# Kernel tuning notes

Hardware: AMD Instinct MI355X
Metric: run time of the kernel (lower is better)

## Reference

```python
import jax, jax.numpy as jnp
import numpy as np

B, D, K = 16384, 256, 1024

def setup_inputs() -> dict:
    key = jax.random.key(0)
    k1, k2 = jax.random.split(key)
    x = jax.random.normal(k1, (B, D), dtype=jnp.float32)
    centers = jax.random.uniform(k2, (K, D), dtype=jnp.float32)  # RandomUniform(0,1)
    betas = jnp.ones((K,), dtype=jnp.float32)
    return {"x": x, "centers": centers, "betas": betas}

def reference(x, centers, betas):
    x_sq = jnp.sum(x * x, axis=-1, keepdims=True)          # [B,1]
    c_sq = jnp.sum(centers * centers, axis=-1)             # [K]
    cross = jnp.einsum('bd,kd->bk', x, centers)            # [B,K]
    diffnorm = x_sq + c_sq[None, :] - 2.0 * cross          # [B,K]
    return jnp.exp(-betas[None, :] * diffnorm)             # [B,K]
```

## Files before the change

### kernel.cpp

```cpp
#include <hip/hip_runtime.h>
#include <stdint.h>

#define D_DIM 256
#define K_CTR 1024
#define B_ROWS 16384
#define BM 32

typedef float f32x4 __attribute__((ext_vector_type(4)));
typedef long long i64x2 __attribute__((ext_vector_type(2)));

static __device__ __forceinline__ unsigned cvt4_fp8(const float4 v) {
    int r = __builtin_amdgcn_cvt_pk_fp8_f32(v.x, v.y, 0, false);
    r = __builtin_amdgcn_cvt_pk_fp8_f32(v.z, v.w, r, true);
    return (unsigned)r;
}

static __device__ __forceinline__ void barrier_lgkm() {
    asm volatile("s_waitcnt lgkmcnt(0)" ::: "memory");
    __builtin_amdgcn_s_barrier();
}

__global__ __launch_bounds__(256) void rbf_prep(const float* __restrict__ centers,
                                                unsigned char* __restrict__ cbf,
                                                float* __restrict__ csq) {
    const int w = threadIdx.x >> 6;
    const int l = threadIdx.x & 63;
    const int c0 = blockIdx.x * 4 + w;
    const float4 v = *reinterpret_cast<const float4*>(centers + c0 * D_DIM + l * 4);
    float s = v.x * v.x + v.y * v.y + v.z * v.z + v.w * v.w;
    const unsigned u = cvt4_fp8(v);
    const unsigned off = (unsigned)((c0 >> 4) * 4096 + (l >> 4) * 1024
                       + (((l >> 1) & 3) * 16 + (c0 & 15)) * 16
                       + ((l >> 3) & 1) * 8 + (l & 1) * 4);
    *reinterpret_cast<unsigned*>(cbf + off) = u;
    #pragma unroll
    for (int off2 = 1; off2 < 64; off2 <<= 1) s += __shfl_xor(s, off2);
    if (l == 0) csq[c0] = s;
}

__global__ __launch_bounds__(512, 4) void rbf_main(const float* __restrict__ x,
                                                   const unsigned char* __restrict__ cbf,
                                                   const float* __restrict__ csq,
                                                   const float* __restrict__ betas,
                                                   float* __restrict__ out) {
    __shared__ __align__(16) unsigned char As[BM * D_DIM];
    __shared__ __align__(16) float obuf[16 * K_CTR];
    __shared__ float xs_lds[BM];

    const int tid = threadIdx.x;
    const int w = tid >> 6;
    const int l = tid & 63;
    const int strip = (blockIdx.x & 7) * 64 + (blockIdx.x >> 3);
    const int row0 = strip * BM;

    #pragma unroll
    for (int i = 0; i < 4; ++i) {
        const int r = i * 8 + w;
        const float4 v = *reinterpret_cast<const float4*>(x + (size_t)(row0 + r) * D_DIM + l * 4);
        float s = v.x * v.x + v.y * v.y + v.z * v.z + v.w * v.w;
        const unsigned u = cvt4_fp8(v);
        const unsigned pos = (unsigned)((l >> 4) * 64 + ((l >> 1) & 3) * 16
                           + ((l >> 3) & 1) * 8 + (l & 1) * 4);
        *reinterpret_cast<unsigned*>(As + r * 256 + (pos ^ ((unsigned)(r & 7) << 4))) = u;
        #pragma unroll
        for (int off = 1; off < 64; off <<= 1) s += __shfl_xor(s, off);
        if (l == 0) xs_lds[r] = s;
    }

    const int hk = l >> 4;
    const int lr = l & 15;
    const unsigned char* bwave = cbf + l * 16;

    i64x2 b0[4], b1[4];
    {
        const unsigned char* bbase = bwave + w * 4096;
        #pragma unroll
        for (int p = 0; p < 4; ++p)
            b0[p] = *reinterpret_cast<const i64x2*>(bbase + p * 1024);
    }
    barrier_lgkm();

    i64x2 a[2][4];
    #pragma unroll
    for (int s = 0; s < 2; ++s) {
        const int r = s * 16 + lr;
        #pragma unroll
        for (int p = 0; p < 4; ++p)
            a[s][p] = *reinterpret_cast<const i64x2*>(
                As + r * 256 + ((unsigned)(p * 64 + hk * 16) ^ ((unsigned)(lr & 7) << 4)));
    }
    const float xsA[2] = { xs_lds[lr], xs_lds[16 + lr] };
    const float LOG2E = 1.4426950408889634f;

    #pragma unroll
    for (int s = 0; s < 2; ++s) {
        #pragma unroll
        for (int ph = 0; ph < 8; ++ph) {
            const int t = s * 8 + ph;
            const i64x2 (&bc)[4] = (t & 1) ? b1 : b0;
            i64x2 (&bn)[4] = (t & 1) ? b0 : b1;

            if (t < 15) {
                const unsigned char* bbase = bwave + (((t + 1) & 7) * 8 + w) * 4096;
                #pragma unroll
                for (int p = 0; p < 4; ++p)
                    bn[p] = *reinterpret_cast<const i64x2*>(bbase + p * 1024);
            }

            f32x4 acc = {};
            #pragma unroll
            for (int p = 0; p < 4; ++p) {
                acc = __builtin_amdgcn_mfma_f32_16x16x32_fp8_fp8(bc[p][0], a[s][p][0], acc, 0, 0, 0);
                acc = __builtin_amdgcn_mfma_f32_16x16x32_fp8_fp8(bc[p][1], a[s][p][1], acc, 0, 0, 0);
            }

            const int cl = ph * 128 + w * 16 + hk * 4;
            const f32x4 cs = *reinterpret_cast<const f32x4*>(csq + cl);
            const f32x4 bt = *reinterpret_cast<const f32x4*>(betas + cl);
            f32x4 rv;
            #pragma unroll
            for (int j = 0; j < 4; ++j) {
                const float btl2 = bt[j] * LOG2E;
                const float c0 = -btl2 * (xsA[s] + cs[j]);
                rv[j] = __builtin_exp2f(__builtin_fmaf(btl2 + btl2, acc[j], c0));
            }
            *reinterpret_cast<f32x4*>(reinterpret_cast<char*>(obuf)
                + lr * 4096 + ((unsigned)(cl * 4) ^ ((unsigned)(lr & 7) << 4))) = rv;
        }
        barrier_lgkm();

        #pragma unroll
        for (int j = 0; j < 2; ++j) {
            const int r = w * 2 + j;
            const unsigned sw = (unsigned)(r & 7) << 4;
            f32x4 sv[4];
            #pragma unroll
            for (int c = 0; c < 4; ++c)
                sv[c] = *reinterpret_cast<const f32x4*>(reinterpret_cast<const char*>(obuf)
                        + r * 4096 + ((unsigned)(l * 16 + c * 1024) ^ sw));
            float* orow = out + (size_t)(row0 + s * 16 + r) * K_CTR;
            #pragma unroll
            for (int c = 0; c < 4; ++c)
                *reinterpret_cast<f32x4*>(orow + c * 256 + l * 4) = sv[c];
        }
        if (s == 0) barrier_lgkm();
    }
}

extern "C" void kernel_launch(void* const* d_in, const int* in_sizes, int n_in,
                              void* d_out, int out_size, void* d_ws, size_t ws_size,
                              hipStream_t stream) {
    const float* x       = (const float*)d_in[0];
    const float* centers = (const float*)d_in[1];
    const float* betas   = (const float*)d_in[2];
    float* out = (float*)d_out;

    unsigned char* cbf = (unsigned char*)d_ws;
    float* csq = (float*)((char*)d_ws + (size_t)K_CTR * D_DIM);

    rbf_prep<<<K_CTR / 4, 256, 0, stream>>>(centers, cbf, csq);
    rbf_main<<<B_ROWS / BM, 512, 0, stream>>>(x, cbf, csq, betas, out);
}
```

Measured before the change: 32.32 us.

## Split work per wave into private column quarters and drop block barriers in epilogue

Each wave now owns one 16-row half and a 256-column quarter of the output instead of sharing column groups across both row halves. That gives each wave a private LDS staging buffer, so the block-wide barriers between compute and store phases go away. Stores are now 8-byte per lane, written every 8 column groups, and MFMA sections are wrapped in s_setprio. The cost is narrower global stores (f32x2) and each wave loading 16 distinct B tiles instead of sharing the prefetch pattern.

```diff
diff --git a/kernel.cpp b/kernel.cpp
--- a/kernel.cpp
+++ b/kernel.cpp
@@ -7,6 +7,7 @@
 #define BM 32
 
 typedef float f32x4 __attribute__((ext_vector_type(4)));
+typedef float f32x2 __attribute__((ext_vector_type(2)));
 typedef long long i64x2 __attribute__((ext_vector_type(2)));
 
 static __device__ __forceinline__ unsigned cvt4_fp8(const float4 v) {
@@ -44,7 +45,7 @@
                                                    const float* __restrict__ betas,
                                                    float* __restrict__ out) {
     __shared__ __align__(16) unsigned char As[BM * D_DIM];
-    __shared__ __align__(16) float obuf[16 * K_CTR];
+    __shared__ __align__(16) float obuf[8][16 * 128];
     __shared__ float xs_lds[BM];
 
     const int tid = threadIdx.x;
@@ -69,81 +70,74 @@
 
     const int hk = l >> 4;
     const int lr = l & 15;
+    const int s = w >> 2;
+    const int q = w & 3;
     const unsigned char* bwave = cbf + l * 16;
 
     i64x2 b0[4], b1[4];
     {
-        const unsigned char* bbase = bwave + w * 4096;
+        const unsigned char* bbase = bwave + (q * 16) * 4096;
         #pragma unroll
         for (int p = 0; p < 4; ++p)
             b0[p] = *reinterpret_cast<const i64x2*>(bbase + p * 1024);
     }
     barrier_lgkm();
 
-    i64x2 a[2][4];
+    i64x2 a[4];
     #pragma unroll
-    for (int s = 0; s < 2; ++s) {
-        const int r = s * 16 + lr;
-        #pragma unroll
-        for (int p = 0; p < 4; ++p)
-            a[s][p] = *reinterpret_cast<const i64x2*>(
-                As + r * 256 + ((unsigned)(p * 64 + hk * 16) ^ ((unsigned)(lr & 7) << 4)));
-    }
-    const float xsA[2] = { xs_lds[lr], xs_lds[16 + lr] };
+    for (int p = 0; p < 4; ++p)
+        a[p] = *reinterpret_cast<const i64x2*>(
+            As + (s * 16 + lr) * 256 + ((unsigned)(p * 64 + hk * 16) ^ ((unsigned)(lr & 7) << 4)));
+    const float xs = xs_lds[s * 16 + lr];
     const float LOG2E = 1.4426950408889634f;
 
+    char* ob = reinterpret_cast<char*>(obuf[w]);
+    float* orow0 = out + (size_t)(row0 + s * 16) * K_CTR + q * 256;
+
     #pragma unroll
-    for (int s = 0; s < 2; ++s) {
+    for (int cg = 0; cg < 16; ++cg) {
+        const int colgrp = q * 16 + cg;
+        const i64x2 (&bc)[4] = (cg & 1) ? b1 : b0;
+        i64x2 (&bn)[4] = (cg & 1) ? b0 : b1;
+
+        if (cg < 15) {
+            const unsigned char* bbase = bwave + (colgrp + 1) * 4096;
+            #pragma unroll
+            for (int p = 0; p < 4; ++p)
+                bn[p] = *reinterpret_cast<const i64x2*>(bbase + p * 1024);
+        }
+
+        f32x4 acc = {};
+        __builtin_amdgcn_s_setprio(1);
         #pragma unroll
-        for (int ph = 0; ph < 8; ++ph) {
-            const int t = s * 8 + ph;
-            const i64x2 (&bc)[4] = (t & 1) ? b1 : b0;
-            i64x2 (&bn)[4] = (t & 1) ? b0 : b1;
+        for (int p = 0; p < 4; ++p) {
+            acc = __builtin_amdgcn_mfma_f32_16x16x32_fp8_fp8(bc[p][0], a[p][0], acc, 0, 0, 0);
+            acc = __builtin_amdgcn_mfma_f32_16x16x32_fp8_fp8(bc[p][1], a[p][1], acc, 0, 0, 0);
+        }
+        __builtin_amdgcn_s_setprio(0);
 
-            if (t < 15) {
-                const unsigned char* bbase = bwave + (((t + 1) & 7) * 8 + w) * 4096;
-                #pragma unroll
-                for (int p = 0; p < 4; ++p)
-                    bn[p] = *reinterpret_cast<const i64x2*>(bbase + p * 1024);
+        const int c0g = colgrp * 16 + hk * 4;
+        const f32x4 cs = *reinterpret_cast<const f32x4*>(csq + c0g);
+        const f32x4 bt = *reinterpret_cast<const f32x4*>(betas + c0g);
+        f32x4 rv;
+        #pragma unroll
+        for (int j = 0; j < 4; ++j) {
+            const float btl2 = bt[j] * LOG2E;
+            const float cc = -btl2 * (xs + cs[j]);
+            rv[j] = __builtin_exp2f(__builtin_fmaf(btl2 + btl2, acc[j], cc));
+        }
+        *reinterpret_cast<f32x4*>(ob + lr * 512
+            + ((unsigned)((cg & 7) * 64 + hk * 16) ^ ((unsigned)(lr & 7) << 4))) = rv;
+
+        if ((cg & 7) == 7) {
+            const int bst = cg >> 3;
+            #pragma unroll
+            for (int r = 0; r < 16; ++r) {
+                const f32x2 v = *reinterpret_cast<const f32x2*>(ob + r * 512
+                        + ((unsigned)(l * 8) ^ ((unsigned)(r & 7) << 4)));
+                *reinterpret_cast<f32x2*>(orow0 + (size_t)r * K_CTR + bst * 128 + l * 2) = v;
             }
-
-            f32x4 acc = {};
-            #pragma unroll
-            for (int p = 0; p < 4; ++p) {
-                acc = __builtin_amdgcn_mfma_f32_16x16x32_fp8_fp8(bc[p][0], a[s][p][0], acc, 0, 0, 0);
-                acc = __builtin_amdgcn_mfma_f32_16x16x32_fp8_fp8(bc[p][1], a[s][p][1], acc, 0, 0, 0);
-            }
-
-            const int cl = ph * 128 + w * 16 + hk * 4;
-            const f32x4 cs = *reinterpret_cast<const f32x4*>(csq + cl);
-            const f32x4 bt = *reinterpret_cast<const f32x4*>(betas + cl);
-            f32x4 rv;
-            #pragma unroll
-            for (int j = 0; j < 4; ++j) {
-                const float btl2 = bt[j] * LOG2E;
-                const float c0 = -btl2 * (xsA[s] + cs[j]);
-                rv[j] = __builtin_exp2f(__builtin_fmaf(btl2 + btl2, acc[j], c0));
-            }
-            *reinterpret_cast<f32x4*>(reinterpret_cast<char*>(obuf)
-                + lr * 4096 + ((unsigned)(cl * 4) ^ ((unsigned)(lr & 7) << 4))) = rv;
         }
-        barrier_lgkm();
-
-        #pragma unroll
-        for (int j = 0; j < 2; ++j) {
-            const int r = w * 2 + j;
-            const unsigned sw = (unsigned)(r & 7) << 4;
-            f32x4 sv[4];
-            #pragma unroll
-            for (int c = 0; c < 4; ++c)
-                sv[c] = *reinterpret_cast<const f32x4*>(reinterpret_cast<const char*>(obuf)
-                        + r * 4096 + ((unsigned)(l * 16 + c * 1024) ^ sw));
-            float* orow = out + (size_t)(row0 + s * 16 + r) * K_CTR;
-            #pragma unroll
-            for (int c = 0; c < 4; ++c)
-                *reinterpret_cast<f32x4*>(orow + c * 256 + l * 4) = sv[c];
-        }
-        if (s == 0) barrier_lgkm();
     }
 }
 
```

Result: no change. 31.69 us (-1.9%).
